# Kernel tuning notes

Measured on AMD Instinct MI355X. Metric: run time of the kernel, lower is better.

## Reference

```python
import jax, jax.numpy as jnp
import numpy as np

N_NODES = 100000
N_EDGES = 1600000
IN_DIM = 128
HID = 128
OUT_DIM = 64
NLP_DIM = 786  # 768 + 11 + 4 + 3
N_LAYERS = 3
N_USERS = 4096
BN_EPS = 1e-5


def setup_inputs() -> dict:
    key = jax.random.key(0)
    ks = jax.random.split(key, 24)
    inp = {
        "x": jax.random.normal(ks[0], (N_NODES, IN_DIM), jnp.float32),
        "nlp_features": jax.random.normal(ks[1], (NLP_DIM,), jnp.float32),
        "edge_index": jax.random.randint(ks[2], (2, N_EDGES), 0, N_NODES),
        "user_indices": jax.random.randint(ks[3], (N_USERS,), 0, N_NODES),
        # input projection
        "W_in": jax.random.normal(ks[4], (IN_DIM, HID), jnp.float32) / np.sqrt(IN_DIM),
        "b_in": jnp.zeros((HID,), jnp.float32),
        # GCN layers (stacked)
        "W_gnn": jax.random.normal(ks[5], (N_LAYERS, HID, HID), jnp.float32) / np.sqrt(HID),
        "b_gnn": jnp.zeros((N_LAYERS, HID), jnp.float32),
        # batchnorm running stats / affine (eval mode)
        "bn_gamma": jnp.ones((N_LAYERS, HID), jnp.float32),
        "bn_beta": jnp.zeros((N_LAYERS, HID), jnp.float32),
        "bn_mean": 0.1 * jax.random.normal(ks[6], (N_LAYERS, HID), jnp.float32),
        "bn_var": 0.5 + jax.random.uniform(ks[7], (N_LAYERS, HID), jnp.float32),
        # node embedding projection
        "W_proj": jax.random.normal(ks[8], (HID, OUT_DIM), jnp.float32) / np.sqrt(HID),
        "b_proj": jnp.zeros((OUT_DIM,), jnp.float32),
        # predictor MLP
        "W1": jax.random.normal(ks[9], (OUT_DIM + NLP_DIM, 256), jnp.float32) / np.sqrt(OUT_DIM + NLP_DIM),
        "b1": jnp.zeros((256,), jnp.float32),
        "W2": jax.random.normal(ks[10], (256, 128), jnp.float32) / np.sqrt(256.0),
        "b2": jnp.zeros((128,), jnp.float32),
        "W3": jax.random.normal(ks[11], (128, 1), jnp.float32) / np.sqrt(128.0),
        "b3": jnp.zeros((1,), jnp.float32),
    }
    return inp


def reference(x, nlp_features, edge_index, user_indices,
              W_in, b_in, W_gnn, b_gnn, bn_gamma, bn_beta, bn_mean, bn_var,
              W_proj, b_proj, W1, b1, W2, b2, W3, b3):
    n = x.shape[0]
    src, dst = edge_index[0], edge_index[1]
    # GCN normalization with self-loops: deg = in-degree + 1
    deg = jax.ops.segment_sum(jnp.ones_like(src, dtype=x.dtype), dst, num_segments=n) + 1.0
    dinv = jax.lax.rsqrt(deg)                      # [N]
    enorm = dinv[src] * dinv[dst]                  # [E]

    h = jax.nn.relu(x @ W_in + b_in)               # [N, HID]
    for i in range(W_gnn.shape[0]):
        hw = h @ W_gnn[i]                          # [N, HID]
        agg = jax.ops.segment_sum(enorm[:, None] * hw[src], dst, num_segments=n)
        agg = agg + (dinv * dinv)[:, None] * hw + b_gnn[i]  # self-loop + bias
        # batchnorm (eval: running stats) + relu; dropout is identity in eval
        hn = (agg - bn_mean[i]) * jax.lax.rsqrt(bn_var[i] + BN_EPS) * bn_gamma[i] + bn_beta[i]
        h = jax.nn.relu(hn)

    emb = h @ W_proj + b_proj                      # [N, OUT_DIM]
    u = emb[user_indices]                          # [B, OUT_DIM]
    nlp = jnp.broadcast_to(nlp_features, (u.shape[0], nlp_features.shape[0]))
    z = jnp.concatenate([u, nlp], axis=1)          # [B, OUT_DIM+NLP_DIM]
    z = jax.nn.relu(z @ W1 + b1)
    z = jax.nn.relu(z @ W2 + b2)
    probs = jax.nn.sigmoid(z @ W3 + b3)
    return probs.squeeze(-1)
```

## Files before the change

kernel.cpp:

```cpp
#include <hip/hip_runtime.h>
#include <math.h>

typedef _Float16 half8_t __attribute__((ext_vector_type(8)));
typedef _Float16 half4_t __attribute__((ext_vector_type(4)));
typedef float    f32x4_t __attribute__((ext_vector_type(4)));


__global__ __launch_bounds__(256) void hist_k(const int* __restrict__ dst, int* __restrict__ cnt,
                                              unsigned short* __restrict__ rank, int E){
  int e = blockIdx.x*256 + threadIdx.x;
  if (e < E) rank[e] = (unsigned short)atomicAdd(&cnt[dst[e]], 1);
}

__global__ __launch_bounds__(256) void blocksum_k(const int* __restrict__ cnt, int* __restrict__ bsum, int N){
  int i = blockIdx.x*256 + threadIdx.x;
  int v = (i < N) ? cnt[i] : 0;
  #pragma unroll
  for (int off = 32; off; off >>= 1) v += __shfl_down(v, off, 64);
  __shared__ int s[4];
  if ((threadIdx.x & 63) == 0) s[threadIdx.x >> 6] = v;
  __syncthreads();
  if (threadIdx.x == 0) bsum[blockIdx.x] = s[0] + s[1] + s[2] + s[3];
}

__global__ __launch_bounds__(512) void scan_small_k(const int* __restrict__ bsum, int* __restrict__ boff, int NB){
  __shared__ int s[512];
  int t = threadIdx.x;
  int v = (t < NB) ? bsum[t] : 0;
  s[t] = v; __syncthreads();
  for (int off = 1; off < 512; off <<= 1){
    int x = (t >= off) ? s[t-off] : 0;
    __syncthreads();
    s[t] += x;
    __syncthreads();
  }
  if (t < NB) boff[t] = s[t] - v;
}

__global__ __launch_bounds__(256) void scan_final_k(const int* __restrict__ cnt, const int* __restrict__ boff,
                                                    int* __restrict__ rowptr,
                                                    float* __restrict__ dinv, int N){
  __shared__ int s[256];
  int t = threadIdx.x;
  int i = blockIdx.x*256 + t;
  int v = (i < N) ? cnt[i] : 0;
  s[t] = v; __syncthreads();
  for (int off = 1; off < 256; off <<= 1){
    int x = (t >= off) ? s[t-off] : 0;
    __syncthreads();
    s[t] += x;
    __syncthreads();
  }
  int excl = s[t] - v + boff[blockIdx.x];
  if (i < N){
    rowptr[i] = excl;
    dinv[i]   = rsqrtf((float)v + 1.0f);
    if (i == N-1) rowptr[N] = excl + v;
  }
}

__global__ __launch_bounds__(256) void fill_k(const int* __restrict__ src, const int* __restrict__ dst,
                                              const int* __restrict__ rowptr,
                                              const unsigned short* __restrict__ rank,
                                              int* __restrict__ col, int E){
  int e2 = (blockIdx.x*256 + threadIdx.x) * 2;
  if (e2 >= E) return;
  int2 d = *(const int2*)&dst[e2];
  int2 s = *(const int2*)&src[e2];
  ushort2 r = *(const ushort2*)&rank[e2];
  col[rowptr[d.x] + r.x] = s.x;
  col[rowptr[d.y] + r.y] = s.y;
}


__global__ __launch_bounds__(256) void prepw_k(const float* __restrict__ Win, const float* __restrict__ Wgnn,
                                               _Float16* __restrict__ Bt){
  int idx = blockIdx.x*256 + threadIdx.x;
  int m = idx >> 14;
  int r = idx & 16383;
  int k = r >> 7, n = r & 127;
  const float* W = (m == 0) ? Win : (Wgnn + (size_t)(m-1)*16384);
  Bt[(size_t)m*16384 + n*128 + k] = (_Float16)W[k*128 + n];
}


template<int AF16, int EPI>
__global__ __launch_bounds__(256) void mgemm_k(const void* __restrict__ Ap, const _Float16* __restrict__ Bt,
                                               const float* __restrict__ bias, const float* __restrict__ dinv,
                                               _Float16* __restrict__ C, int M){
  __shared__ _Float16 As[128*128];
  __shared__ _Float16 Bs[128*128];
  const int tid = threadIdx.x;
  const int m0 = blockIdx.x * 128;

  {
    int n = tid >> 1, kb = (tid & 1) * 64;
    const half8_t* srcb = (const half8_t*)(Bt + n*128 + kb);
    #pragma unroll
    for (int q = 0; q < 8; ++q){
      uint32_t byte = (uint32_t)(n*256 + kb*2 + q*16) ^ (uint32_t)((n & 7) << 4);
      *(half8_t*)((char*)Bs + byte) = srcb[q];
    }
  }
  {
    int rr = tid >> 1, kb = (tid & 1) * 64;
    int row = m0 + rr; if (row >= M) row = M - 1;
    if (AF16){
      const half8_t* srca = (const half8_t*)((const _Float16*)Ap + (size_t)row*128 + kb);
      #pragma unroll
      for (int q = 0; q < 8; ++q){
        uint32_t byte = (uint32_t)(rr*256 + kb*2 + q*16) ^ (uint32_t)((rr & 7) << 4);
        *(half8_t*)((char*)As + byte) = srca[q];
      }
    } else {
      const float4* srca = (const float4*)((const float*)Ap + (size_t)row*128 + kb);
      #pragma unroll
      for (int q = 0; q < 8; ++q){
        float4 f0 = srca[2*q], f1 = srca[2*q+1];
        half8_t h;
        h[0]=(_Float16)f0.x; h[1]=(_Float16)f0.y; h[2]=(_Float16)f0.z; h[3]=(_Float16)f0.w;
        h[4]=(_Float16)f1.x; h[5]=(_Float16)f1.y; h[6]=(_Float16)f1.z; h[7]=(_Float16)f1.w;
        uint32_t byte = (uint32_t)(rr*256 + kb*2 + q*16) ^ (uint32_t)((rr & 7) << 4);
        *(half8_t*)((char*)As + byte) = h;
      }
    }
  }
  __syncthreads();

  const int w = tid >> 6, lane = tid & 63;
  const int l15 = lane & 15, lq = lane >> 4;

  f32x4_t acc[2][8];
  #pragma unroll
  for (int rg = 0; rg < 2; ++rg)
    #pragma unroll
    for (int cg = 0; cg < 8; ++cg)
      acc[rg][cg] = (f32x4_t){0.f,0.f,0.f,0.f};

  #pragma unroll
  for (int ks = 0; ks < 4; ++ks){
    half8_t a[2], b[8];
    #pragma unroll
    for (int rg = 0; rg < 2; ++rg){
      int row = w*32 + rg*16 + l15;
      uint32_t byte = (uint32_t)(row*256 + (ks*32 + lq*8)*2) ^ (uint32_t)((row & 7) << 4);
      a[rg] = *(const half8_t*)((const char*)As + byte);
    }
    #pragma unroll
    for (int cg = 0; cg < 8; ++cg){
      int coln = cg*16 + l15;
      uint32_t byte = (uint32_t)(coln*256 + (ks*32 + lq*8)*2) ^ (uint32_t)((coln & 7) << 4);
      b[cg] = *(const half8_t*)((const char*)Bs + byte);
    }
    #pragma unroll
    for (int rg = 0; rg < 2; ++rg)
      #pragma unroll
      for (int cg = 0; cg < 8; ++cg)
        acc[rg][cg] = __builtin_amdgcn_mfma_f32_16x16x32_f16(a[rg], b[cg], acc[rg][cg], 0, 0, 0);
  }

  float bl[8];
  if (EPI == 0){
    #pragma unroll
    for (int cg = 0; cg < 8; ++cg) bl[cg] = bias[cg*16 + l15];
  }

  #pragma unroll
  for (int rg = 0; rg < 2; ++rg){
    #pragma unroll
    for (int r = 0; r < 4; ++r){
      int grow = m0 + w*32 + rg*16 + lq*4 + r;
      if (grow < M){
        if (EPI == 1){
          float di = dinv[grow];
          #pragma unroll
          for (int cg = 0; cg < 8; ++cg)
            C[(size_t)grow*128 + cg*16 + l15] = (_Float16)(di * acc[rg][cg][r]);
        } else {
          #pragma unroll
          for (int cg = 0; cg < 8; ++cg){
            float v = acc[rg][cg][r] + bl[cg];
            C[(size_t)grow*128 + cg*16 + l15] = (_Float16)fmaxf(v, 0.f);
          }
        }
      }
    }
  }
}


template<int ACT>
__global__ __launch_bounds__(256) void gemm_k(const float* __restrict__ A, const float* __restrict__ B,
                                              const float* __restrict__ bias, float* __restrict__ C,
                                              int M, int N, int K){
  __shared__ float As[16][68];
  __shared__ float Bs[16][68];
  int tid = threadIdx.x;
  int m0 = blockIdx.x * 64, n0 = blockIdx.y * 64;
  int ty = tid >> 4, tx = tid & 15;
  int lm = tid >> 2, lkq = tid & 3;
  int lk = tid >> 4, ln4 = tid & 15;
  int arow = m0 + lm; if (arow >= M) arow = M - 1;

  float acc[4][4] = {{0.f}};

  for (int k0 = 0; k0 < K; k0 += 16){
    float4 av = *(const float4*)&A[(size_t)arow*K + k0 + lkq*4];
    float4 bv = *(const float4*)&B[(size_t)(k0+lk)*N + n0 + ln4*4];
    As[lkq*4+0][lm] = av.x; As[lkq*4+1][lm] = av.y; As[lkq*4+2][lm] = av.z; As[lkq*4+3][lm] = av.w;
    *(float4*)&Bs[lk][ln4*4] = bv;
    __syncthreads();
    #pragma unroll
    for (int kk = 0; kk < 16; ++kk){
      const float4 a = *(const float4*)&As[kk][ty*4];
      const float4 b = *(const float4*)&Bs[kk][tx*4];
      acc[0][0] += a.x*b.x; acc[0][1] += a.x*b.y; acc[0][2] += a.x*b.z; acc[0][3] += a.x*b.w;
      acc[1][0] += a.y*b.x; acc[1][1] += a.y*b.y; acc[1][2] += a.y*b.z; acc[1][3] += a.y*b.w;
      acc[2][0] += a.z*b.x; acc[2][1] += a.z*b.y; acc[2][2] += a.z*b.z; acc[2][3] += a.z*b.w;
      acc[3][0] += a.w*b.x; acc[3][1] += a.w*b.y; acc[3][2] += a.w*b.z; acc[3][3] += a.w*b.w;
    }
    __syncthreads();
  }

  float bv0 = 0.f, bv1 = 0.f, bv2 = 0.f, bv3 = 0.f;
  if (bias){
    const float4 b4 = *(const float4*)&bias[n0 + tx*4];
    bv0 = b4.x; bv1 = b4.y; bv2 = b4.z; bv3 = b4.w;
  }
  #pragma unroll
  for (int i = 0; i < 4; ++i){
    int r = m0 + ty*4 + i;
    if (r < M){
      float4 o;
      o.x = acc[i][0] + bv0; o.y = acc[i][1] + bv1; o.z = acc[i][2] + bv2; o.w = acc[i][3] + bv3;
      if (ACT == 1){ o.x = fmaxf(o.x,0.f); o.y = fmaxf(o.y,0.f); o.z = fmaxf(o.z,0.f); o.w = fmaxf(o.w,0.f); }
      *(float4*)&C[(size_t)r*N + n0 + tx*4] = o;
    }
  }
}


__global__ __launch_bounds__(256) void agg_k(const _Float16* __restrict__ hws, _Float16* __restrict__ hout,
                                             const int* __restrict__ rowptr, const int* __restrict__ col,
                                             const float* __restrict__ dinv,
                                             const float* __restrict__ bgnn, const float* __restrict__ gamma,
                                             const float* __restrict__ beta, const float* __restrict__ mean,
                                             const float* __restrict__ var, int N){
  int n = (blockIdx.x * blockDim.x + threadIdx.x) >> 6;
  if (n >= N) return;
  int lane = threadIdx.x & 63;
  int half = lane >> 5;
  int sl   = lane & 31;
  int f    = sl * 4;
  int beg = rowptr[n], end = rowptr[n+1];
  const _Float16* hwsf = hws + f;

  half4_t H0 = {0,0,0,0}, H1 = {0,0,0,0}, H2 = {0,0,0,0}, H3 = {0,0,0,0};
  half4_t H4 = {0,0,0,0}, H5 = {0,0,0,0}, H6 = {0,0,0,0}, H7 = {0,0,0,0};

  int j = beg + half;
  for (; j + 14 < end; j += 16){
    int s0 = col[j],    s1 = col[j+2],  s2 = col[j+4],  s3 = col[j+6];
    int s4 = col[j+8],  s5 = col[j+10], s6 = col[j+12], s7 = col[j+14];
    H0 += *(const half4_t*)&hwsf[(size_t)s0*128];
    H1 += *(const half4_t*)&hwsf[(size_t)s1*128];
    H2 += *(const half4_t*)&hwsf[(size_t)s2*128];
    H3 += *(const half4_t*)&hwsf[(size_t)s3*128];
    H4 += *(const half4_t*)&hwsf[(size_t)s4*128];
    H5 += *(const half4_t*)&hwsf[(size_t)s5*128];
    H6 += *(const half4_t*)&hwsf[(size_t)s6*128];
    H7 += *(const half4_t*)&hwsf[(size_t)s7*128];
  }
  for (; j + 6 < end; j += 8){
    int s0 = col[j], s1 = col[j+2], s2 = col[j+4], s3 = col[j+6];
    H0 += *(const half4_t*)&hwsf[(size_t)s0*128];
    H1 += *(const half4_t*)&hwsf[(size_t)s1*128];
    H2 += *(const half4_t*)&hwsf[(size_t)s2*128];
    H3 += *(const half4_t*)&hwsf[(size_t)s3*128];
  }
  for (; j < end; j += 2){
    int s0 = col[j];
    H0 += *(const half4_t*)&hwsf[(size_t)s0*128];
  }

  float4 A0;
  A0.x = ((float)H0[0] + (float)H1[0]) + ((float)H2[0] + (float)H3[0])
       + ((float)H4[0] + (float)H5[0]) + ((float)H6[0] + (float)H7[0]);
  A0.y = ((float)H0[1] + (float)H1[1]) + ((float)H2[1] + (float)H3[1])
       + ((float)H4[1] + (float)H5[1]) + ((float)H6[1] + (float)H7[1]);
  A0.z = ((float)H0[2] + (float)H1[2]) + ((float)H2[2] + (float)H3[2])
       + ((float)H4[2] + (float)H5[2]) + ((float)H6[2] + (float)H7[2]);
  A0.w = ((float)H0[3] + (float)H1[3]) + ((float)H2[3] + (float)H3[3])
       + ((float)H4[3] + (float)H5[3]) + ((float)H6[3] + (float)H7[3]);

  A0.x += __shfl_xor(A0.x, 32, 64);
  A0.y += __shfl_xor(A0.y, 32, 64);
  A0.z += __shfl_xor(A0.z, 32, 64);
  A0.w += __shfl_xor(A0.w, 32, 64);

  if (half == 0){
    float di = dinv[n];
    const half4_t hv = *(const half4_t*)&hwsf[(size_t)n*128];
    const float4 bg = *(const float4*)&bgnn[f];
    const float4 gm = *(const float4*)&gamma[f];
    const float4 bt = *(const float4*)&beta[f];
    const float4 mn = *(const float4*)&mean[f];
    const float4 vr = *(const float4*)&var[f];
    float o0 = (di*(A0.x + (float)hv[0]) + bg.x - mn.x) * (gm.x * rsqrtf(vr.x + 1e-5f)) + bt.x;
    float o1 = (di*(A0.y + (float)hv[1]) + bg.y - mn.y) * (gm.y * rsqrtf(vr.y + 1e-5f)) + bt.y;
    float o2 = (di*(A0.z + (float)hv[2]) + bg.z - mn.z) * (gm.z * rsqrtf(vr.z + 1e-5f)) + bt.z;
    float o3 = (di*(A0.w + (float)hv[3]) + bg.w - mn.w) * (gm.w * rsqrtf(vr.w + 1e-5f)) + bt.w;
    half4_t o;
    o[0] = (_Float16)fmaxf(o0, 0.f);
    o[1] = (_Float16)fmaxf(o1, 0.f);
    o[2] = (_Float16)fmaxf(o2, 0.f);
    o[3] = (_Float16)fmaxf(o3, 0.f);
    *(half4_t*)&hout[(size_t)n*128 + f] = o;
  }
}


__global__ __launch_bounds__(256) void gather_k(const _Float16* __restrict__ h, const int* __restrict__ uidx,
                                                float* __restrict__ uh, int B){
  int g = blockIdx.x*256 + threadIdx.x;
  if (g >= B*128) return;
  int i = g >> 7, f = g & 127;
  uh[g] = (float)h[(size_t)uidx[i]*128 + f];
}

__global__ __launch_bounds__(256) void initc1_k(const float* __restrict__ b1, float* __restrict__ c1){
  c1[threadIdx.x] = b1[threadIdx.x];
}

__global__ __launch_bounds__(256) void c1acc_k(const float* __restrict__ nlp, const float* __restrict__ W1,
                                               float* __restrict__ c1, int NLP){
  int c = threadIdx.x;
  int d0 = blockIdx.x * 16;
  int d1 = d0 + 16 < NLP ? d0 + 16 : NLP;
  float acc = 0.f;
  for (int d = d0; d < d1; ++d)
    acc += nlp[d] * W1[(size_t)(64 + d) * 256 + c];
  atomicAdd(&c1[c], acc);
}

__global__ __launch_bounds__(256) void head_k(const float* __restrict__ z2, const float* __restrict__ W3,
                                              const float* __restrict__ b3, float* __restrict__ out, int B){
  int gid = blockIdx.x * blockDim.x + threadIdx.x;
  int u = gid >> 6, l = gid & 63;
  if (u >= B) return;
  float v = z2[(size_t)u*128 + l] * W3[l] + z2[(size_t)u*128 + 64 + l] * W3[64 + l];
  #pragma unroll
  for (int off = 32; off; off >>= 1) v += __shfl_down(v, off, 64);
  if (l == 0) out[u] = 1.f / (1.f + expf(-(v + b3[0])));
}


static void launch_gemm(int act, const float* A, const float* Bm, const float* bias, float* C,
                        int M, int N, int K, hipStream_t s){
  dim3 g((M + 63) / 64, N / 64);
  if (act) hipLaunchKernelGGL((gemm_k<1>), g, dim3(256), 0, s, A, Bm, bias, C, M, N, K);
  else     hipLaunchKernelGGL((gemm_k<0>), g, dim3(256), 0, s, A, Bm, bias, C, M, N, K);
}

extern "C" void kernel_launch(void* const* d_in, const int* in_sizes, int n_in,
                              void* d_out, int out_size, void* d_ws, size_t ws_size,
                              hipStream_t stream){
  const float* x     = (const float*)d_in[0];
  const float* nlp   = (const float*)d_in[1];
  const int*   eidx  = (const int*)  d_in[2];
  const int*   uidx  = (const int*)  d_in[3];
  const float* W_in  = (const float*)d_in[4];
  const float* b_in  = (const float*)d_in[5];
  const float* W_gnn = (const float*)d_in[6];
  const float* b_gnn = (const float*)d_in[7];
  const float* gam   = (const float*)d_in[8];
  const float* bet   = (const float*)d_in[9];
  const float* mean  = (const float*)d_in[10];
  const float* var   = (const float*)d_in[11];
  const float* Wproj = (const float*)d_in[12];
  const float* bproj = (const float*)d_in[13];
  const float* W1    = (const float*)d_in[14];
  const float* b1    = (const float*)d_in[15];
  const float* W2    = (const float*)d_in[16];
  const float* b2    = (const float*)d_in[17];
  const float* W3    = (const float*)d_in[18];
  const float* b3    = (const float*)d_in[19];
  float* out = (float*)d_out;

  const int N   = in_sizes[0] / 128;
  const int E   = in_sizes[2] / 2;
  const int B   = in_sizes[3];
  const int NLP = in_sizes[1];
  const int HID = 128;

  char* p = (char*)d_ws;
  auto carve = [&](size_t bytes) -> void* {
    void* q = (void*)p;
    p += (bytes + 255) & ~(size_t)255;
    return q;
  };
  int*            cnt    = (int*)           carve((size_t)N * 4);
  int*            rowptr = (int*)           carve((size_t)(N + 1) * 4);
  unsigned short* rank   = (unsigned short*)carve((size_t)E * 2);
  int*            bsum   = (int*)           carve(512 * 4);
  int*            boff   = (int*)           carve(512 * 4);
  float*          dinv   = (float*)         carve((size_t)N * 4);
  int*            col    = (int*)           carve((size_t)E * 4);
  _Float16*       Bt     = (_Float16*)      carve((size_t)4 * 128 * 128 * 2);
  _Float16*       h      = (_Float16*)      carve((size_t)N * HID * 2);
  _Float16*       hws    = (_Float16*)      carve((size_t)N * HID * 2);
  float*          uh     = (float*)         carve((size_t)B * HID * 4);
  float*          embu   = (float*)         carve((size_t)B * 64 * 4);
  float*          z1     = (float*)         carve((size_t)B * 256 * 4);
  float*          z2     = (float*)         carve((size_t)B * 128 * 4);
  float*          c1     = (float*)         carve(256 * 4);

  const int* src = eidx;
  const int* dst = eidx + E;

  const int NB = (N + 255) / 256;
  const int GB = (N + 127) / 128;

  hipMemsetAsync(cnt, 0, (size_t)N * 4, stream);
  hipLaunchKernelGGL(hist_k, dim3((E + 255) / 256), dim3(256), 0, stream, dst, cnt, rank, E);
  hipLaunchKernelGGL(blocksum_k, dim3(NB), dim3(256), 0, stream, cnt, bsum, N);
  hipLaunchKernelGGL(scan_small_k, dim3(1), dim3(512), 0, stream, bsum, boff, NB);
  hipLaunchKernelGGL(scan_final_k, dim3(NB), dim3(256), 0, stream, cnt, boff, rowptr, dinv, N);
  hipLaunchKernelGGL(fill_k, dim3((E/2 + 255) / 256), dim3(256), 0, stream, src, dst, rowptr, rank, col, E);

  hipLaunchKernelGGL(prepw_k, dim3(256), dim3(256), 0, stream, W_in, W_gnn, Bt);

  hipLaunchKernelGGL((mgemm_k<0,0>), dim3(GB), dim3(256), 0, stream,
                     (const void*)x, Bt, b_in, (const float*)nullptr, h, N);

  for (int i = 0; i < 3; ++i){
    hipLaunchKernelGGL((mgemm_k<1,1>), dim3(GB), dim3(256), 0, stream,
                       (const void*)h, Bt + (size_t)(i+1)*16384, (const float*)nullptr, dinv, hws, N);
    hipLaunchKernelGGL(agg_k, dim3((N * 64 + 255) / 256), dim3(256), 0, stream,
                       hws, h, rowptr, col, dinv,
                       b_gnn + i * 128, gam + i * 128, bet + i * 128, mean + i * 128, var + i * 128, N);
  }

  hipLaunchKernelGGL(gather_k, dim3((B * 128 + 255) / 256), dim3(256), 0, stream, h, uidx, uh, B);
  hipLaunchKernelGGL(initc1_k, dim3(1), dim3(256), 0, stream, b1, c1);
  hipLaunchKernelGGL(c1acc_k, dim3((NLP + 15) / 16), dim3(256), 0, stream, nlp, W1, c1, NLP);

  launch_gemm(0, uh, Wproj, bproj, embu, B, 64, 128, stream);
  launch_gemm(1, embu, W1, c1, z1, B, 256, 64, stream);
  launch_gemm(1, z1, W2, b2, z2, B, 128, 256, stream);
  hipLaunchKernelGGL(head_k, dim3((B * 64 + 255) / 256), dim3(256), 0, stream, z2, W3, b3, out, B);
}
```

Baseline: 559.5 us.

## Load GEMM operands directly from global, prescale column offsets, split agg neighbors contiguously

The dense GEMM no longer stages A and B tiles through LDS and instead loads MFMA fragments straight from global memory, which drops the shared-memory copy and the barrier but gives up coalesced, reused loads. The CSR column array now holds byte offsets (src*256), which removes per-edge multiplies in aggregation. Each half-wave now walks a contiguous half of the neighbor list instead of interleaved edges. Partial sums are also reduced in fp16 before converting to float, which slightly changes precision.

```diff
diff --git a/kernel.cpp b/kernel.cpp
--- a/kernel.cpp
+++ b/kernel.cpp
@@ -62,14 +62,14 @@
 __global__ __launch_bounds__(256) void fill_k(const int* __restrict__ src, const int* __restrict__ dst,
                                               const int* __restrict__ rowptr,
                                               const unsigned short* __restrict__ rank,
-                                              int* __restrict__ col, int E){
+                                              int* __restrict__ colb, int E){
   int e2 = (blockIdx.x*256 + threadIdx.x) * 2;
   if (e2 >= E) return;
   int2 d = *(const int2*)&dst[e2];
   int2 s = *(const int2*)&src[e2];
   ushort2 r = *(const ushort2*)&rank[e2];
-  col[rowptr[d.x] + r.x] = s.x;
-  col[rowptr[d.y] + r.y] = s.y;
+  colb[rowptr[d.x] + r.x] = s.x * 256;
+  colb[rowptr[d.y] + r.y] = s.y * 256;
 }
 
 
@@ -88,70 +88,45 @@
 __global__ __launch_bounds__(256) void mgemm_k(const void* __restrict__ Ap, const _Float16* __restrict__ Bt,
                                                const float* __restrict__ bias, const float* __restrict__ dinv,
                                                _Float16* __restrict__ C, int M){
-  __shared__ _Float16 As[128*128];
-  __shared__ _Float16 Bs[128*128];
   const int tid = threadIdx.x;
   const int m0 = blockIdx.x * 128;
-
-  {
-    int n = tid >> 1, kb = (tid & 1) * 64;
-    const half8_t* srcb = (const half8_t*)(Bt + n*128 + kb);
-    #pragma unroll
-    for (int q = 0; q < 8; ++q){
-      uint32_t byte = (uint32_t)(n*256 + kb*2 + q*16) ^ (uint32_t)((n & 7) << 4);
-      *(half8_t*)((char*)Bs + byte) = srcb[q];
-    }
-  }
-  {
-    int rr = tid >> 1, kb = (tid & 1) * 64;
-    int row = m0 + rr; if (row >= M) row = M - 1;
-    if (AF16){
-      const half8_t* srca = (const half8_t*)((const _Float16*)Ap + (size_t)row*128 + kb);
-      #pragma unroll
-      for (int q = 0; q < 8; ++q){
-        uint32_t byte = (uint32_t)(rr*256 + kb*2 + q*16) ^ (uint32_t)((rr & 7) << 4);
-        *(half8_t*)((char*)As + byte) = srca[q];
-      }
-    } else {
-      const float4* srca = (const float4*)((const float*)Ap + (size_t)row*128 + kb);
-      #pragma unroll
-      for (int q = 0; q < 8; ++q){
-        float4 f0 = srca[2*q], f1 = srca[2*q+1];
+  const int w = tid >> 6, lane = tid & 63;
+  const int l15 = lane & 15, lq = lane >> 4;
+
+  f32x4_t acc[2][8];
+  #pragma unroll
+  for (int rg = 0; rg < 2; ++rg)
+    #pragma unroll
+    for (int cg = 0; cg < 8; ++cg)
+      acc[rg][cg] = (f32x4_t){0.f,0.f,0.f,0.f};
+
+  int arow[2];
+  #pragma unroll
+  for (int rg = 0; rg < 2; ++rg){
+    int r = m0 + w*32 + rg*16 + l15;
+    arow[rg] = (r < M) ? r : (M - 1);
+  }
+
+  #pragma unroll
+  for (int ks = 0; ks < 4; ++ks){
+    const int kb = ks*32 + lq*8;
+    half8_t a[2], b[8];
+    #pragma unroll
+    for (int rg = 0; rg < 2; ++rg){
+      if (AF16){
+        a[rg] = *(const half8_t*)((const _Float16*)Ap + (size_t)arow[rg]*128 + kb);
+      } else {
+        const float* af = (const float*)Ap + (size_t)arow[rg]*128 + kb;
+        float4 f0 = *(const float4*)af, f1 = *(const float4*)(af + 4);
         half8_t h;
         h[0]=(_Float16)f0.x; h[1]=(_Float16)f0.y; h[2]=(_Float16)f0.z; h[3]=(_Float16)f0.w;
         h[4]=(_Float16)f1.x; h[5]=(_Float16)f1.y; h[6]=(_Float16)f1.z; h[7]=(_Float16)f1.w;
-        uint32_t byte = (uint32_t)(rr*256 + kb*2 + q*16) ^ (uint32_t)((rr & 7) << 4);
-        *(half8_t*)((char*)As + byte) = h;
+        a[rg] = h;
       }
     }
-  }
-  __syncthreads();
-
-  const int w = tid >> 6, lane = tid & 63;
-  const int l15 = lane & 15, lq = lane >> 4;
-
-  f32x4_t acc[2][8];
-  #pragma unroll
-  for (int rg = 0; rg < 2; ++rg)
     #pragma unroll
     for (int cg = 0; cg < 8; ++cg)
-      acc[rg][cg] = (f32x4_t){0.f,0.f,0.f,0.f};
-
-  #pragma unroll
-  for (int ks = 0; ks < 4; ++ks){
-    half8_t a[2], b[8];
-    #pragma unroll
-    for (int rg = 0; rg < 2; ++rg){
-      int row = w*32 + rg*16 + l15;
-      uint32_t byte = (uint32_t)(row*256 + (ks*32 + lq*8)*2) ^ (uint32_t)((row & 7) << 4);
-      a[rg] = *(const half8_t*)((const char*)As + byte);
-    }
-    #pragma unroll
-    for (int cg = 0; cg < 8; ++cg){
-      int coln = cg*16 + l15;
-      uint32_t byte = (uint32_t)(coln*256 + (ks*32 + lq*8)*2) ^ (uint32_t)((coln & 7) << 4);
-      b[cg] = *(const half8_t*)((const char*)Bs + byte);
-    }
+      b[cg] = *(const half8_t*)(Bt + (size_t)(cg*16 + l15)*128 + kb);
     #pragma unroll
     for (int rg = 0; rg < 2; ++rg)
       #pragma unroll
@@ -241,7 +216,7 @@
 
 
 __global__ __launch_bounds__(256) void agg_k(const _Float16* __restrict__ hws, _Float16* __restrict__ hout,
-                                             const int* __restrict__ rowptr, const int* __restrict__ col,
+                                             const int* __restrict__ rowptr, const int* __restrict__ colb,
                                              const float* __restrict__ dinv,
                                              const float* __restrict__ bgnn, const float* __restrict__ gamma,
                                              const float* __restrict__ beta, const float* __restrict__ mean,
@@ -253,45 +228,44 @@
   int sl   = lane & 31;
   int f    = sl * 4;
   int beg = rowptr[n], end = rowptr[n+1];
-  const _Float16* hwsf = hws + f;
+  int mid = beg + ((end - beg + 1) >> 1);
+  int jb  = half ? mid : beg;
+  int je  = half ? end : mid;
+  const char* base = (const char*)hws + (size_t)f * 2;
 
   half4_t H0 = {0,0,0,0}, H1 = {0,0,0,0}, H2 = {0,0,0,0}, H3 = {0,0,0,0};
   half4_t H4 = {0,0,0,0}, H5 = {0,0,0,0}, H6 = {0,0,0,0}, H7 = {0,0,0,0};
 
-  int j = beg + half;
-  for (; j + 14 < end; j += 16){
-    int s0 = col[j],    s1 = col[j+2],  s2 = col[j+4],  s3 = col[j+6];
-    int s4 = col[j+8],  s5 = col[j+10], s6 = col[j+12], s7 = col[j+14];
-    H0 += *(const half4_t*)&hwsf[(size_t)s0*128];
-    H1 += *(const half4_t*)&hwsf[(size_t)s1*128];
-    H2 += *(const half4_t*)&hwsf[(size_t)s2*128];
-    H3 += *(const half4_t*)&hwsf[(size_t)s3*128];
-    H4 += *(const half4_t*)&hwsf[(size_t)s4*128];
-    H5 += *(const half4_t*)&hwsf[(size_t)s5*128];
-    H6 += *(const half4_t*)&hwsf[(size_t)s6*128];
-    H7 += *(const half4_t*)&hwsf[(size_t)s7*128];
-  }
-  for (; j + 6 < end; j += 8){
-    int s0 = col[j], s1 = col[j+2], s2 = col[j+4], s3 = col[j+6];
-    H0 += *(const half4_t*)&hwsf[(size_t)s0*128];
-    H1 += *(const half4_t*)&hwsf[(size_t)s1*128];
-    H2 += *(const half4_t*)&hwsf[(size_t)s2*128];
-    H3 += *(const half4_t*)&hwsf[(size_t)s3*128];
-  }
-  for (; j < end; j += 2){
-    int s0 = col[j];
-    H0 += *(const half4_t*)&hwsf[(size_t)s0*128];
-  }
+  int j = jb;
+  for (; j + 8 <= je; j += 8){
+    int o0 = colb[j],   o1 = colb[j+1], o2 = colb[j+2], o3 = colb[j+3];
+    int o4 = colb[j+4], o5 = colb[j+5], o6 = colb[j+6], o7 = colb[j+7];
+    H0 += *(const half4_t*)(base + o0);
+    H1 += *(const half4_t*)(base + o1);
+    H2 += *(const half4_t*)(base + o2);
+    H3 += *(const half4_t*)(base + o3);
+    H4 += *(const half4_t*)(base + o4);
+    H5 += *(const half4_t*)(base + o5);
+    H6 += *(const half4_t*)(base + o6);
+    H7 += *(const half4_t*)(base + o7);
+  }
+  for (; j + 4 <= je; j += 4){
+    int o0 = colb[j], o1 = colb[j+1], o2 = colb[j+2], o3 = colb[j+3];
+    H0 += *(const half4_t*)(base + o0);
+    H1 += *(const half4_t*)(base + o1);
+    H2 += *(const half4_t*)(base + o2);
+    H3 += *(const half4_t*)(base + o3);
+  }
+  for (; j < je; ++j){
+    H0 += *(const half4_t*)(base + colb[j]);
+  }
+
+  H0 += H1; H2 += H3; H4 += H5; H6 += H7;
+  H0 += H2; H4 += H6;
+  H0 += H4;
 
   float4 A0;
-  A0.x = ((float)H0[0] + (float)H1[0]) + ((float)H2[0] + (float)H3[0])
-       + ((float)H4[0] + (float)H5[0]) + ((float)H6[0] + (float)H7[0]);
-  A0.y = ((float)H0[1] + (float)H1[1]) + ((float)H2[1] + (float)H3[1])
-       + ((float)H4[1] + (float)H5[1]) + ((float)H6[1] + (float)H7[1]);
-  A0.z = ((float)H0[2] + (float)H1[2]) + ((float)H2[2] + (float)H3[2])
-       + ((float)H4[2] + (float)H5[2]) + ((float)H6[2] + (float)H7[2]);
-  A0.w = ((float)H0[3] + (float)H1[3]) + ((float)H2[3] + (float)H3[3])
-       + ((float)H4[3] + (float)H5[3]) + ((float)H6[3] + (float)H7[3]);
+  A0.x = (float)H0[0]; A0.y = (float)H0[1]; A0.z = (float)H0[2]; A0.w = (float)H0[3];
 
   A0.x += __shfl_xor(A0.x, 32, 64);
   A0.y += __shfl_xor(A0.y, 32, 64);
@@ -300,7 +274,7 @@
 
   if (half == 0){
     float di = dinv[n];
-    const half4_t hv = *(const half4_t*)&hwsf[(size_t)n*128];
+    const half4_t hv = *(const half4_t*)(base + (size_t)n*256);
     const float4 bg = *(const float4*)&bgnn[f];
     const float4 gm = *(const float4*)&gamma[f];
     const float4 bt = *(const float4*)&beta[f];
@@ -405,7 +379,7 @@
   int*            bsum   = (int*)           carve(512 * 4);
   int*            boff   = (int*)           carve(512 * 4);
   float*          dinv   = (float*)         carve((size_t)N * 4);
-  int*            col    = (int*)           carve((size_t)E * 4);
+  int*            colb   = (int*)           carve((size_t)E * 4);
   _Float16*       Bt     = (_Float16*)      carve((size_t)4 * 128 * 128 * 2);
   _Float16*       h      = (_Float16*)      carve((size_t)N * HID * 2);
   _Float16*       hws    = (_Float16*)      carve((size_t)N * HID * 2);
@@ -426,7 +400,7 @@
   hipLaunchKernelGGL(blocksum_k, dim3(NB), dim3(256), 0, stream, cnt, bsum, N);
   hipLaunchKernelGGL(scan_small_k, dim3(1), dim3(512), 0, stream, bsum, boff, NB);
   hipLaunchKernelGGL(scan_final_k, dim3(NB), dim3(256), 0, stream, cnt, boff, rowptr, dinv, N);
-  hipLaunchKernelGGL(fill_k, dim3((E/2 + 255) / 256), dim3(256), 0, stream, src, dst, rowptr, rank, col, E);
+  hipLaunchKernelGGL(fill_k, dim3((E/2 + 255) / 256), dim3(256), 0, stream, src, dst, rowptr, rank, colb, E);
 
   hipLaunchKernelGGL(prepw_k, dim3(256), dim3(256), 0, stream, W_in, W_gnn, Bt);
 
@@ -437,7 +411,7 @@
     hipLaunchKernelGGL((mgemm_k<1,1>), dim3(GB), dim3(256), 0, stream,
                        (const void*)h, Bt + (size_t)(i+1)*16384, (const float*)nullptr, dinv, hws, N);
     hipLaunchKernelGGL(agg_k, dim3((N * 64 + 255) / 256), dim3(256), 0, stream,
-                       hws, h, rowptr, col, dinv,
+                       hws, h, rowptr, colb, dinv,
                        b_gnn + i * 128, gam + i * 128, bet + i * 128, mean + i * 128, var + i * 128, N);
   }
 
```

After: 588.9 us. +5.2%, slower.

## Split aggregation across feature slices with edge-parallel lanes and prescaled column offsets

Applied to the files above, without the earlier changes.

The aggregation kernel is restructured so each wave handles one node and one 32-byte feature slice (8 blocks per group of 4 nodes). The 64 lanes split into 32 edge slots times 2 half-slices, each loading 16 bytes, with a shuffle-xor tree reduction at the end. Column indices are prescaled to byte offsets in fill_k and read with nontemporal loads, which removes address multiplication. This gives more parallelism per node for low-degree graphs, but each column index is now read 8 times and the reduction has more shuffle steps.

```diff
diff --git a/kernel.cpp b/kernel.cpp
--- a/kernel.cpp
+++ b/kernel.cpp
@@ -62,14 +62,14 @@
 __global__ __launch_bounds__(256) void fill_k(const int* __restrict__ src, const int* __restrict__ dst,
                                               const int* __restrict__ rowptr,
                                               const unsigned short* __restrict__ rank,
-                                              int* __restrict__ col, int E){
+                                              int* __restrict__ colb, int E){
   int e2 = (blockIdx.x*256 + threadIdx.x) * 2;
   if (e2 >= E) return;
   int2 d = *(const int2*)&dst[e2];
   int2 s = *(const int2*)&src[e2];
   ushort2 r = *(const ushort2*)&rank[e2];
-  col[rowptr[d.x] + r.x] = s.x;
-  col[rowptr[d.y] + r.y] = s.y;
+  colb[rowptr[d.x] + r.x] = s.x * 256;
+  colb[rowptr[d.y] + r.y] = s.y * 256;
 }
 
 
@@ -240,82 +240,50 @@
 }
 
 
-__global__ __launch_bounds__(256) void agg_k(const _Float16* __restrict__ hws, _Float16* __restrict__ hout,
-                                             const int* __restrict__ rowptr, const int* __restrict__ col,
-                                             const float* __restrict__ dinv,
-                                             const float* __restrict__ bgnn, const float* __restrict__ gamma,
-                                             const float* __restrict__ beta, const float* __restrict__ mean,
-                                             const float* __restrict__ var, int N){
-  int n = (blockIdx.x * blockDim.x + threadIdx.x) >> 6;
+__device__ inline half8_t shflx16(half8_t v, int m){
+  union { half8_t h; int i[4]; } u; u.h = v;
+  u.i[0] = __shfl_xor(u.i[0], m, 64);
+  u.i[1] = __shfl_xor(u.i[1], m, 64);
+  u.i[2] = __shfl_xor(u.i[2], m, 64);
+  u.i[3] = __shfl_xor(u.i[3], m, 64);
+  return u.h;
+}
+
+__global__ __launch_bounds__(256) void agg8_k(const _Float16* __restrict__ hws, _Float16* __restrict__ hout,
+                                              const int* __restrict__ rowptr, const int* __restrict__ colb,
+                                              const float* __restrict__ dinv,
+                                              const float* __restrict__ bgnn, const float* __restrict__ gamma,
+                                              const float* __restrict__ beta, const float* __restrict__ mean,
+                                              const float* __restrict__ var, int N){
+  const int fq = blockIdx.x & 7;
+  const int n  = (blockIdx.x >> 3) * 4 + (threadIdx.x >> 6);
   if (n >= N) return;
-  int lane = threadIdx.x & 63;
-  int half = lane >> 5;
-  int sl   = lane & 31;
-  int f    = sl * 4;
-  int beg = rowptr[n], end = rowptr[n+1];
-  const _Float16* hwsf = hws + f;
-
-  half4_t H0 = {0,0,0,0}, H1 = {0,0,0,0}, H2 = {0,0,0,0}, H3 = {0,0,0,0};
-  half4_t H4 = {0,0,0,0}, H5 = {0,0,0,0}, H6 = {0,0,0,0}, H7 = {0,0,0,0};
-
-  int j = beg + half;
-  for (; j + 14 < end; j += 16){
-    int s0 = col[j],    s1 = col[j+2],  s2 = col[j+4],  s3 = col[j+6];
-    int s4 = col[j+8],  s5 = col[j+10], s6 = col[j+12], s7 = col[j+14];
-    H0 += *(const half4_t*)&hwsf[(size_t)s0*128];
-    H1 += *(const half4_t*)&hwsf[(size_t)s1*128];
-    H2 += *(const half4_t*)&hwsf[(size_t)s2*128];
-    H3 += *(const half4_t*)&hwsf[(size_t)s3*128];
-    H4 += *(const half4_t*)&hwsf[(size_t)s4*128];
-    H5 += *(const half4_t*)&hwsf[(size_t)s5*128];
-    H6 += *(const half4_t*)&hwsf[(size_t)s6*128];
-    H7 += *(const half4_t*)&hwsf[(size_t)s7*128];
-  }
-  for (; j + 6 < end; j += 8){
-    int s0 = col[j], s1 = col[j+2], s2 = col[j+4], s3 = col[j+6];
-    H0 += *(const half4_t*)&hwsf[(size_t)s0*128];
-    H1 += *(const half4_t*)&hwsf[(size_t)s1*128];
-    H2 += *(const half4_t*)&hwsf[(size_t)s2*128];
-    H3 += *(const half4_t*)&hwsf[(size_t)s3*128];
-  }
-  for (; j < end; j += 2){
-    int s0 = col[j];
-    H0 += *(const half4_t*)&hwsf[(size_t)s0*128];
-  }
-
-  float4 A0;
-  A0.x = ((float)H0[0] + (float)H1[0]) + ((float)H2[0] + (float)H3[0])
-       + ((float)H4[0] + (float)H5[0]) + ((float)H6[0] + (float)H7[0]);
-  A0.y = ((float)H0[1] + (float)H1[1]) + ((float)H2[1] + (float)H3[1])
-       + ((float)H4[1] + (float)H5[1]) + ((float)H6[1] + (float)H7[1]);
-  A0.z = ((float)H0[2] + (float)H1[2]) + ((float)H2[2] + (float)H3[2])
-       + ((float)H4[2] + (float)H5[2]) + ((float)H6[2] + (float)H7[2]);
-  A0.w = ((float)H0[3] + (float)H1[3]) + ((float)H2[3] + (float)H3[3])
-       + ((float)H4[3] + (float)H5[3]) + ((float)H6[3] + (float)H7[3]);
-
-  A0.x += __shfl_xor(A0.x, 32, 64);
-  A0.y += __shfl_xor(A0.y, 32, 64);
-  A0.z += __shfl_xor(A0.z, 32, 64);
-  A0.w += __shfl_xor(A0.w, 32, 64);
-
-  if (half == 0){
+  const int lane = threadIdx.x & 63;
+  const int slot = lane >> 1, hb = lane & 1;
+  const int beg = rowptr[n], end = rowptr[n+1];
+  const char* base = (const char*)hws + fq*32 + hb*16;
+
+  half8_t H = {0,0,0,0,0,0,0,0};
+  for (int j = beg + slot; j < end; j += 32){
+    int off = __builtin_nontemporal_load(&colb[j]);
+    H += *(const half8_t*)(base + off);
+  }
+  #pragma unroll
+  for (int m = 2; m < 64; m <<= 1) H += shflx16(H, m);
+
+  if (slot == 0){
     float di = dinv[n];
-    const half4_t hv = *(const half4_t*)&hwsf[(size_t)n*128];
-    const float4 bg = *(const float4*)&bgnn[f];
-    const float4 gm = *(const float4*)&gamma[f];
-    const float4 bt = *(const float4*)&beta[f];
-    const float4 mn = *(const float4*)&mean[f];
-    const float4 vr = *(const float4*)&var[f];
-    float o0 = (di*(A0.x + (float)hv[0]) + bg.x - mn.x) * (gm.x * rsqrtf(vr.x + 1e-5f)) + bt.x;
-    float o1 = (di*(A0.y + (float)hv[1]) + bg.y - mn.y) * (gm.y * rsqrtf(vr.y + 1e-5f)) + bt.y;
-    float o2 = (di*(A0.z + (float)hv[2]) + bg.z - mn.z) * (gm.z * rsqrtf(vr.z + 1e-5f)) + bt.z;
-    float o3 = (di*(A0.w + (float)hv[3]) + bg.w - mn.w) * (gm.w * rsqrtf(vr.w + 1e-5f)) + bt.w;
-    half4_t o;
-    o[0] = (_Float16)fmaxf(o0, 0.f);
-    o[1] = (_Float16)fmaxf(o1, 0.f);
-    o[2] = (_Float16)fmaxf(o2, 0.f);
-    o[3] = (_Float16)fmaxf(o3, 0.f);
-    *(half4_t*)&hout[(size_t)n*128 + f] = o;
+    const half8_t hv = *(const half8_t*)(base + (size_t)n*256);
+    const int f0 = fq*16 + hb*8;
+    half8_t o;
+    #pragma unroll
+    for (int i = 0; i < 8; ++i){
+      int f = f0 + i;
+      float a = di * ((float)H[i] + (float)hv[i]) + bgnn[f] - mean[f];
+      float v = a * (gamma[f] * rsqrtf(var[f] + 1e-5f)) + beta[f];
+      o[i] = (_Float16)fmaxf(v, 0.f);
+    }
+    *(half8_t*)((char*)hout + (size_t)n*256 + fq*32 + hb*16) = o;
   }
 }
 
@@ -405,7 +373,7 @@
   int*            bsum   = (int*)           carve(512 * 4);
   int*            boff   = (int*)           carve(512 * 4);
   float*          dinv   = (float*)         carve((size_t)N * 4);
-  int*            col    = (int*)           carve((size_t)E * 4);
+  int*            colb   = (int*)           carve((size_t)E * 4);
   _Float16*       Bt     = (_Float16*)      carve((size_t)4 * 128 * 128 * 2);
   _Float16*       h      = (_Float16*)      carve((size_t)N * HID * 2);
   _Float16*       hws    = (_Float16*)      carve((size_t)N * HID * 2);
@@ -426,18 +394,19 @@
   hipLaunchKernelGGL(blocksum_k, dim3(NB), dim3(256), 0, stream, cnt, bsum, N);
   hipLaunchKernelGGL(scan_small_k, dim3(1), dim3(512), 0, stream, bsum, boff, NB);
   hipLaunchKernelGGL(scan_final_k, dim3(NB), dim3(256), 0, stream, cnt, boff, rowptr, dinv, N);
-  hipLaunchKernelGGL(fill_k, dim3((E/2 + 255) / 256), dim3(256), 0, stream, src, dst, rowptr, rank, col, E);
+  hipLaunchKernelGGL(fill_k, dim3((E/2 + 255) / 256), dim3(256), 0, stream, src, dst, rowptr, rank, colb, E);
 
   hipLaunchKernelGGL(prepw_k, dim3(256), dim3(256), 0, stream, W_in, W_gnn, Bt);
 
   hipLaunchKernelGGL((mgemm_k<0,0>), dim3(GB), dim3(256), 0, stream,
                      (const void*)x, Bt, b_in, (const float*)nullptr, h, N);
 
+  const int AGB = ((N + 3) / 4) * 8;
   for (int i = 0; i < 3; ++i){
     hipLaunchKernelGGL((mgemm_k<1,1>), dim3(GB), dim3(256), 0, stream,
                        (const void*)h, Bt + (size_t)(i+1)*16384, (const float*)nullptr, dinv, hws, N);
-    hipLaunchKernelGGL(agg_k, dim3((N * 64 + 255) / 256), dim3(256), 0, stream,
-                       hws, h, rowptr, col, dinv,
+    hipLaunchKernelGGL(agg8_k, dim3(AGB), dim3(256), 0, stream,
+                       hws, h, rowptr, colb, dinv,
                        b_gnn + i * 128, gam + i * 128, bet + i * 128, mean + i * 128, var + i * 128, N);
   }
 
```

Result: slower. 1.528 ms (+173.1%).
